# Performance work log

Hardware: AMD Instinct MI355X
Metric: run time of the kernel (lower is better)

Reference implementation:

```python
import jax, jax.numpy as jnp
from jax import lax
import numpy as np

L = 256       # regions
M = 8         # inputs
HID = 1024    # MLP hidden
T = 2048      # t_eval points
DT = 0.05
ALPHA_RES = 0.1
KAPPA, GAMMA, TAU, HALPHA, RHO, V0 = 0.65, 0.41, 0.98, 0.32, 0.34, 0.04


def setup_inputs() -> dict:
    key = jax.random.key(0)
    ks = jax.random.split(key, 8)
    A = -jnp.eye(L, dtype=jnp.float32) + 0.05 * jax.random.normal(ks[0], (L, L), jnp.float32) / np.sqrt(L)
    B = 0.01 * jax.random.normal(ks[1], (M, L, L), jnp.float32) / np.sqrt(L)
    C = 0.1 * jax.random.normal(ks[2], (L, M), jnp.float32)
    W1 = jax.random.normal(ks[3], (HID, L + M), jnp.float32) / np.sqrt(L + M)
    b1 = jnp.zeros((HID,), jnp.float32)
    W2 = jax.random.normal(ks[4], (L, HID), jnp.float32) / np.sqrt(HID)
    b2 = jnp.zeros((L,), jnp.float32)
    # u sampled on half-step grid: stages of step i use rows 2i, 2i+1, 2i+1, 2i+2
    u_seq = 0.1 * jax.random.uniform(ks[5], (2 * (T - 1) + 1, M), jnp.float32)
    t_eval = jnp.arange(T, dtype=jnp.float32) * DT
    return {"A": A, "B": B, "C": C, "W1": W1, "b1": b1, "W2": W2, "b2": b2,
            "u_seq": u_seq, "t_eval": t_eval}


def _simulate(A, B, C, W1, b1, W2, b2, u_seq, t_eval):
    l = A.shape[0]

    def dyn(state, u_t):
        z = state[:l]
        s_, f_, v_, q_ = state[l:].reshape(4, l)
        # residual MLP on concat(z, u)
        zu = jnp.concatenate([z, u_t])
        res = W2 @ jnp.tanh(W1 @ zu + b1) + b2
        # bilinear neuronal dynamics + residual
        dz = A @ z + jnp.einsum('m,mij,j->i', u_t, B, z) + C @ u_t + ALPHA_RES * res
        # hemodynamic balloon model
        ds = z - KAPPA * s_ - GAMMA * (f_ - 1.0)
        df = s_
        fv = v_ ** (1.0 / HALPHA)        # outflow v^(1/alpha)
        dv = (f_ - fv) / TAU
        E = 1.0 - (1.0 - RHO) ** (1.0 / f_)  # oxygen extraction
        dq = (f_ * E / RHO - fv * q_ / v_) / TAU
        return jnp.concatenate([dz, ds, df, dv, dq])

    def rk4_step(state, inp):
        h, u0, um, u1 = inp
        k1 = dyn(state, u0)
        k2 = dyn(state + 0.5 * h * k1, um)
        k3 = dyn(state + 0.5 * h * k2, um)
        k4 = dyn(state + h * k3, u1)
        nxt = state + (h / 6.0) * (k1 + 2.0 * k2 + 2.0 * k3 + k4)
        return nxt, nxt

    s0 = jnp.concatenate([jnp.zeros((2 * l,), A.dtype), jnp.ones((3 * l,), A.dtype)])  # z=0,s=0,f=v=q=1
    hs = t_eval[1:] - t_eval[:-1]                  # [T-1]
    u0 = u_seq[0:-2:2]; um = u_seq[1:-1:2]; u1 = u_seq[2::2]
    _, states = lax.scan(rk4_step, s0, (hs, u0, um, u1))
    S = jnp.concatenate([s0[None, :], states], axis=0)  # [T, 5l]
    v = S[:, 3 * l:4 * l]
    q = S[:, 4 * l:5 * l]
    k1b, k2b, k3b = 7.0 * RHO, 2.0, 2.0 * RHO - 0.2
    Y = V0 * (k1b * (1.0 - q) + k2b * (1.0 - q / v) + k3b * (1.0 - v))  # [T, l]
    return S, Y


def reference(A, B, C, W1, b1, W2, b2, u_seq, t_eval):
    return _simulate(A, B, C, W1, b1, W2, b2, u_seq, t_eval)
```

## Files before the change

### kernel.cpp

```cpp
#include <hip/hip_runtime.h>
#include <cmath>

#define LN 256
#define MM 8
#define HIDN 1024
#define NSTEP 2047
#define NWG 32
#define TPB 256
#define W1R 32
#define GR 8
#define ZUN (LN+MM)

#define KAPPA 0.65f
#define GAMMA 0.41f
#define TAUC 0.98f
#define INV_HALPHA 3.125f
#define RHOC 0.34f
#define V0C 0.04f
#define ALPHA 0.1f
#define LOG2_1MRHO (-0.5994620717f)

#define OFF_W1 0
#define N_W1 (W1R*ZUN)
#define OFF_W2 (OFF_W1+N_W1)
#define N_W2 (W1R*LN)
#define OFF_A (OFF_W2+N_W2)
#define N_A (GR*LN)
#define OFF_B (OFF_A+N_A)
#define N_B (MM*GR*LN)
#define OFF_C (OFF_B+N_B)
#define N_C (GR*MM)
#define OFF_B1 (OFF_C+N_C)
#define N_B1 (W1R)
#define OFF_B2 (OFF_B1+N_B1)
#define N_B2 (GR)
#define OFF_ZU (OFF_B2+N_B2)
#define N_ZU (ZUN)
#define OFF_H (OFF_ZU+N_ZU)
#define N_H (W1R)
#define OFF_P (OFF_H+N_H)
#define N_P (GR)
#define SMEM_FLOATS (OFF_P+N_P)
#define SMEM_BYTES (SMEM_FLOATS*4)

#define WS_PART_OFF 4096
#define FLG_STRIDE 16

__global__ void dcm_init(unsigned int* flg) {
  flg[threadIdx.x] = 0u;
}

__global__ void __launch_bounds__(TPB, 1) dcm_kernel(
    const float* __restrict__ Ag, const float* __restrict__ Bg,
    const float* __restrict__ Cg, const float* __restrict__ W1g,
    const float* __restrict__ b1g, const float* __restrict__ W2g,
    const float* __restrict__ b2g, const float* __restrict__ Ug,
    const float* __restrict__ Tg, float* __restrict__ outg,
    float* __restrict__ part, unsigned int* __restrict__ flg)
{
  extern __shared__ float sm[];
  const int wg = blockIdx.x, tid = threadIdx.x;
  float* w1s = sm + OFF_W1;
  float* w2s = sm + OFF_W2;
  float* as_ = sm + OFF_A;
  float* bs_ = sm + OFF_B;
  float* cs_ = sm + OFF_C;
  float* b1s = sm + OFF_B1;
  float* b2s = sm + OFF_B2;
  float* zu  = sm + OFF_ZU;
  float* hsh = sm + OFF_H;
  float* pts = sm + OFF_P;

  for (int i = tid; i < N_W1; i += TPB) {
    int r = i / ZUN, k = i - r * ZUN;
    w1s[i] = W1g[(wg * W1R + r) * ZUN + k];
  }
  for (int i = tid; i < N_W2; i += TPB) {
    int c = i >> 8, r = i & (LN - 1);
    w2s[i] = W2g[r * HIDN + wg * W1R + c];
  }
  for (int i = tid; i < N_A; i += TPB) {
    int r = i >> 8, k = i & (LN - 1);
    as_[i] = Ag[(wg * GR + r) * LN + k];
  }
  for (int i = tid; i < N_B; i += TPB) {
    int m = i / (GR * LN); int rem = i - m * GR * LN;
    int r = rem >> 8, k = rem & (LN - 1);
    bs_[i] = Bg[(m * LN + wg * GR + r) * LN + k];
  }
  for (int i = tid; i < N_C; i += TPB) {
    int r = i >> 3, m = i & 7;
    cs_[i] = Cg[(wg * GR + r) * MM + m];
  }
  for (int i = tid; i < N_B1; i += TPB) b1s[i] = b1g[wg * W1R + i];
  for (int i = tid; i < N_B2; i += TPB) b2s[i] = b2g[wg * GR + i];

  float zb = 0.f, sb = 0.f, fb = 1.f, vb = 1.f, qb = 1.f;
  zu[tid] = 0.f;

  if (wg == 0) {
    outg[tid] = 0.f;
    outg[LN + tid] = 0.f;
    outg[2 * LN + tid] = 1.f;
    outg[3 * LN + tid] = 1.f;
    outg[4 * LN + tid] = 1.f;
    outg[(size_t)2048 * 1280 + tid] = 0.f;
  }

  int pp = 0;

  for (int t = 0; t < NSTEP; ++t) {
    float hstep = Tg[t + 1] - Tg[t];
    float zst = zb, sst = sb, fst = fb, vst = vb, qst = qb;
    float kz = 0.f, ks = 0.f, kf = 0.f, kv = 0.f, kq = 0.f;

    for (int st = 0; st < 4; ++st) {
      int usel = (st == 0) ? (2 * t) : (st == 3) ? (2 * t + 2) : (2 * t + 1);
      if (tid < MM) zu[LN + tid] = Ug[usel * MM + tid];
      __syncthreads();

      float uu[MM];
      #pragma unroll
      for (int m = 0; m < MM; ++m) uu[m] = zu[LN + m];

      {
        int row = tid >> 3, sub = tid & 7;
        const float* wrow = w1s + row * ZUN + sub * 33;
        const float* zrow = zu + sub * 33;
        float acc = 0.f;
        #pragma unroll
        for (int j = 0; j < 33; ++j) acc += wrow[j] * zrow[j];
        acc += __shfl_xor(acc, 1);
        acc += __shfl_xor(acc, 2);
        acc += __shfl_xor(acc, 4);
        if (sub == 0) hsh[row] = tanhf(acc + b1s[row]);
      }
      {
        int grow = tid >> 5, gsub = tid & 31;
        const float* arow = as_ + grow * LN;
        float ga = 0.f;
        #pragma unroll
        for (int j = 0; j < 8; ++j) {
          int k = gsub + 32 * j;
          float w = arow[k];
          #pragma unroll
          for (int m = 0; m < MM; ++m) w += uu[m] * bs_[(m * GR + grow) * LN + k];
          ga += w * zu[k];
        }
        ga += __shfl_xor(ga, 1);
        ga += __shfl_xor(ga, 2);
        ga += __shfl_xor(ga, 4);
        ga += __shfl_xor(ga, 8);
        ga += __shfl_xor(ga, 16);
        if (gsub == 0) {
          float cu = 0.f;
          #pragma unroll
          for (int m = 0; m < MM; ++m) cu += cs_[grow * MM + m] * uu[m];
          pts[grow] = ga + cu + ALPHA * b2s[grow];
        }
      }
      __syncthreads();

      float pr;
      {
        float a2 = 0.f;
        #pragma unroll 8
        for (int c = 0; c < W1R; ++c) a2 += w2s[c * LN + tid] * hsh[c];
        pr = ALPHA * a2;
        int rl = tid - wg * GR;
        if (rl >= 0 && rl < GR) pr += pts[rl];
      }
      __hip_atomic_store(&part[((pp * NWG) + wg) * LN + tid], pr,
                         __ATOMIC_RELAXED, __HIP_MEMORY_SCOPE_AGENT);

      float ds = zst - KAPPA * sst - GAMMA * (fst - 1.f);
      float df = sst;
      float fv = exp2f(INV_HALPHA * log2f(vst));
      float dv = (fst - fv) / TAUC;
      float E  = 1.f - exp2f(LOG2_1MRHO / fst);
      float dq = (fst * E / RHOC - fv * qst / vst) / TAUC;

      __syncthreads();

      unsigned e = (unsigned)(4 * t + st + 1);
      if (tid == 0)
        __hip_atomic_store(&flg[wg * FLG_STRIDE], e,
                           __ATOMIC_RELAXED, __HIP_MEMORY_SCOPE_AGENT);

      {
        const unsigned* fp_ = &flg[(tid & 31) * FLG_STRIDE];
        for (;;) {
          unsigned v = __hip_atomic_load(fp_, __ATOMIC_RELAXED,
                                         __HIP_MEMORY_SCOPE_AGENT);
          if (__ballot(v >= e) == 0xFFFFFFFFFFFFFFFFull) break;
        }
      }

      float dz = 0.f;
      #pragma unroll
      for (int g = 0; g < NWG; ++g)
        dz += __hip_atomic_load(&part[(pp * NWG + g) * LN + tid],
                                __ATOMIC_RELAXED, __HIP_MEMORY_SCOPE_AGENT);

      float wk = (st == 0 || st == 3) ? 1.f : 2.f;
      kz += wk * dz; ks += wk * ds; kf += wk * df; kv += wk * dv; kq += wk * dq;

      if (st < 3) {
        float c = (st == 2) ? hstep : 0.5f * hstep;
        zst = zb + c * dz; sst = sb + c * ds; fst = fb + c * df;
        vst = vb + c * dv; qst = qb + c * dq;
        zu[tid] = zst;
      }
      pp ^= 1;
    }

    float h6 = hstep * (1.f / 6.f);
    zb += h6 * kz; sb += h6 * ks; fb += h6 * kf; vb += h6 * kv; qb += h6 * kq;
    zu[tid] = zb;

    if ((t & (NWG - 1)) == wg) {
      size_t ro = (size_t)(t + 1) * 1280;
      outg[ro + tid] = zb;
      outg[ro + LN + tid] = sb;
      outg[ro + 2 * LN + tid] = fb;
      outg[ro + 3 * LN + tid] = vb;
      outg[ro + 4 * LN + tid] = qb;
      float yv = V0C * (2.38f * (1.f - qb) + 2.f * (1.f - qb / vb) + 0.48f * (1.f - vb));
      outg[(size_t)2048 * 1280 + (size_t)(t + 1) * LN + tid] = yv;
    }
  }
}

extern "C" void kernel_launch(void* const* d_in, const int* in_sizes, int n_in,
                              void* d_out, int out_size, void* d_ws, size_t ws_size,
                              hipStream_t stream) {
  const float* Ag  = (const float*)d_in[0];
  const float* Bg  = (const float*)d_in[1];
  const float* Cg  = (const float*)d_in[2];
  const float* W1g = (const float*)d_in[3];
  const float* b1g = (const float*)d_in[4];
  const float* W2g = (const float*)d_in[5];
  const float* b2g = (const float*)d_in[6];
  const float* Ug  = (const float*)d_in[7];
  const float* Tg  = (const float*)d_in[8];
  float* outg = (float*)d_out;

  unsigned int* flg = (unsigned int*)d_ws;
  float* part = (float*)((char*)d_ws + WS_PART_OFF);

  hipFuncSetAttribute((const void*)dcm_kernel,
                      hipFuncAttributeMaxDynamicSharedMemorySize, SMEM_BYTES);

  hipLaunchKernelGGL(dcm_init, dim3(1), dim3(512), 0, stream, flg);
  hipLaunchKernelGGL(dcm_kernel, dim3(NWG), dim3(TPB), SMEM_BYTES, stream,
                     Ag, Bg, Cg, W1g, b1g, W2g, b2g, Ug, Tg, outg, part, flg);
}
```

Before: 27.70 ms.

## Pack epoch tags with partial sums to replace flag barrier

The inter-workgroup exchange now writes each partial sum together with its step epoch as a single 64-bit atomic store into a double-buffered array. Consumers poll the data slots directly until every tag matches, which removes the separate flag store, the extra __syncthreads, the ballot spin and the second round of loads. The flag-reset init kernel is dropped, and the three u rows for each step are loaded into registers once per step. In exchange, every thread polls 32 remote 64-bit slots, and correctness relies on stale workspace contents never carrying a matching epoch.

```diff
diff --git a/kernel.cpp b/kernel.cpp
--- a/kernel.cpp
+++ b/kernel.cpp
@@ -43,12 +43,6 @@
 #define SMEM_FLOATS (OFF_P+N_P)
 #define SMEM_BYTES (SMEM_FLOATS*4)
 
-#define WS_PART_OFF 4096
-#define FLG_STRIDE 16
-
-__global__ void dcm_init(unsigned int* flg) {
-  flg[threadIdx.x] = 0u;
-}
 
 __global__ void __launch_bounds__(TPB, 1) dcm_kernel(
     const float* __restrict__ Ag, const float* __restrict__ Bg,
@@ -56,7 +50,7 @@
     const float* __restrict__ b1g, const float* __restrict__ W2g,
     const float* __restrict__ b2g, const float* __restrict__ Ug,
     const float* __restrict__ Tg, float* __restrict__ outg,
-    float* __restrict__ part, unsigned int* __restrict__ flg)
+    unsigned long long* __restrict__ ex)
 {
   extern __shared__ float sm[];
   const int wg = blockIdx.x, tid = threadIdx.x;
@@ -107,16 +101,20 @@
     outg[(size_t)2048 * 1280 + tid] = 0.f;
   }
 
-  int pp = 0;
-
   for (int t = 0; t < NSTEP; ++t) {
     float hstep = Tg[t + 1] - Tg[t];
     float zst = zb, sst = sb, fst = fb, vst = vb, qst = qb;
     float kz = 0.f, ks = 0.f, kf = 0.f, kv = 0.f, kq = 0.f;
 
+    float u0r = 0.f, umr = 0.f, u1r = 0.f;
+    if (tid < MM) {
+      u0r = Ug[(2 * t) * MM + tid];
+      umr = Ug[(2 * t + 1) * MM + tid];
+      u1r = Ug[(2 * t + 2) * MM + tid];
+    }
+
     for (int st = 0; st < 4; ++st) {
-      int usel = (st == 0) ? (2 * t) : (st == 3) ? (2 * t + 2) : (2 * t + 1);
-      if (tid < MM) zu[LN + tid] = Ug[usel * MM + tid];
+      if (tid < MM) zu[LN + tid] = (st == 0) ? u0r : (st == 3) ? u1r : umr;
       __syncthreads();
 
       float uu[MM];
@@ -170,7 +168,11 @@
         int rl = tid - wg * GR;
         if (rl >= 0 && rl < GR) pr += pts[rl];
       }
-      __hip_atomic_store(&part[((pp * NWG) + wg) * LN + tid], pr,
+
+      const unsigned e = (unsigned)(4 * t + st + 1);
+      unsigned long long* exb = ex + (size_t)(e & 1) * (NWG * LN);
+      __hip_atomic_store(&exb[wg * LN + tid],
+                         ((unsigned long long)e << 32) | (unsigned long long)__float_as_uint(pr),
                          __ATOMIC_RELAXED, __HIP_MEMORY_SCOPE_AGENT);
 
       float ds = zst - KAPPA * sst - GAMMA * (fst - 1.f);
@@ -180,27 +182,24 @@
       float E  = 1.f - exp2f(LOG2_1MRHO / fst);
       float dq = (fst * E / RHOC - fv * qst / vst) / TAUC;
 
-      __syncthreads();
-
-      unsigned e = (unsigned)(4 * t + st + 1);
-      if (tid == 0)
-        __hip_atomic_store(&flg[wg * FLG_STRIDE], e,
-                           __ATOMIC_RELAXED, __HIP_MEMORY_SCOPE_AGENT);
-
-      {
-        const unsigned* fp_ = &flg[(tid & 31) * FLG_STRIDE];
-        for (;;) {
-          unsigned v = __hip_atomic_load(fp_, __ATOMIC_RELAXED,
-                                         __HIP_MEMORY_SCOPE_AGENT);
-          if (__ballot(v >= e) == 0xFFFFFFFFFFFFFFFFull) break;
-        }
+      unsigned long long vv[NWG];
+      unsigned done = 0u;
+      while (done != 0xFFFFFFFFu) {
+        #pragma unroll
+        for (int g = 0; g < NWG; ++g)
+          if (!(done & (1u << g)))
+            vv[g] = __hip_atomic_load(&exb[g * LN + tid],
+                                      __ATOMIC_RELAXED, __HIP_MEMORY_SCOPE_AGENT);
+        #pragma unroll
+        for (int g = 0; g < NWG; ++g)
+          if (!(done & (1u << g)))
+            if ((unsigned)(vv[g] >> 32) == e) done |= (1u << g);
       }
 
       float dz = 0.f;
       #pragma unroll
       for (int g = 0; g < NWG; ++g)
-        dz += __hip_atomic_load(&part[(pp * NWG + g) * LN + tid],
-                                __ATOMIC_RELAXED, __HIP_MEMORY_SCOPE_AGENT);
+        dz += __uint_as_float((unsigned)vv[g]);
 
       float wk = (st == 0 || st == 3) ? 1.f : 2.f;
       kz += wk * dz; ks += wk * ds; kf += wk * df; kv += wk * dv; kq += wk * dq;
@@ -211,7 +210,6 @@
         vst = vb + c * dv; qst = qb + c * dq;
         zu[tid] = zst;
       }
-      pp ^= 1;
     }
 
     float h6 = hstep * (1.f / 6.f);
@@ -245,13 +243,11 @@
   const float* Tg  = (const float*)d_in[8];
   float* outg = (float*)d_out;
 
-  unsigned int* flg = (unsigned int*)d_ws;
-  float* part = (float*)((char*)d_ws + WS_PART_OFF);
+  unsigned long long* ex = (unsigned long long*)d_ws;
 
   hipFuncSetAttribute((const void*)dcm_kernel,
                       hipFuncAttributeMaxDynamicSharedMemorySize, SMEM_BYTES);
 
-  hipLaunchKernelGGL(dcm_init, dim3(1), dim3(512), 0, stream, flg);
   hipLaunchKernelGGL(dcm_kernel, dim3(NWG), dim3(TPB), SMEM_BYTES, stream,
-                     Ag, Bg, Cg, W1g, b1g, W2g, b2g, Ug, Tg, outg, part, flg);
+                     Ag, Bg, Cg, W1g, b1g, W2g, b2g, Ug, Tg, outg, ex);
 }
```

Measured after the change: 43.60 ms. +57.4%, slower.

## Use per-wavefront release flags and double-buffered z to drop a block barrier

Applied to the files above, without the earlier changes.

Each wavefront now publishes its own release flag and waits only on the matching wavefront flags of the other workgroups. This removes the block-wide __syncthreads before the inter-workgroup handshake. The z/u shared buffer is double-buffered so stage writes cannot race with reads from the previous stage. The u loads are hoisted out of the stage loop and the partial-sum reduction is split into two accumulators. A deadman spin limit is added, which can silently break out of the wait and produce wrong results if a workgroup stalls for too long.

```diff
diff --git a/kernel.cpp b/kernel.cpp
--- a/kernel.cpp
+++ b/kernel.cpp
@@ -19,6 +19,8 @@
 #define V0C 0.04f
 #define ALPHA 0.1f
 #define LOG2_1MRHO (-0.5994620717f)
+
+#define DEADMAN (1<<14)
 
 #define OFF_W1 0
 #define N_W1 (W1R*ZUN)
@@ -34,20 +36,18 @@
 #define N_B1 (W1R)
 #define OFF_B2 (OFF_B1+N_B1)
 #define N_B2 (GR)
-#define OFF_ZU (OFF_B2+N_B2)
-#define N_ZU (ZUN)
-#define OFF_H (OFF_ZU+N_ZU)
-#define N_H (W1R)
-#define OFF_P (OFF_H+N_H)
-#define N_P (GR)
-#define SMEM_FLOATS (OFF_P+N_P)
+#define OFF_ZA (OFF_B2+N_B2)
+#define OFF_ZB (OFF_ZA+ZUN)
+#define OFF_H (OFF_ZB+ZUN)
+#define OFF_P (OFF_H+W1R)
+#define SMEM_FLOATS (OFF_P+GR)
 #define SMEM_BYTES (SMEM_FLOATS*4)
 
-#define WS_PART_OFF 4096
-#define FLG_STRIDE 16
-
-__global__ void dcm_init(unsigned int* flg) {
-  flg[threadIdx.x] = 0u;
+#define WS_PART_OFF 8192
+#define FSTR 16
+
+__global__ void dcm_init(unsigned* wflag) {
+  for (int i = threadIdx.x; i < NWG * 4 * FSTR; i += 256) wflag[i] = 0u;
 }
 
 __global__ void __launch_bounds__(TPB, 1) dcm_kernel(
@@ -56,10 +56,11 @@
     const float* __restrict__ b1g, const float* __restrict__ W2g,
     const float* __restrict__ b2g, const float* __restrict__ Ug,
     const float* __restrict__ Tg, float* __restrict__ outg,
-    float* __restrict__ part, unsigned int* __restrict__ flg)
+    float* __restrict__ part, unsigned* __restrict__ wflag)
 {
   extern __shared__ float sm[];
   const int wg = blockIdx.x, tid = threadIdx.x;
+  const int myw = tid >> 6;
   float* w1s = sm + OFF_W1;
   float* w2s = sm + OFF_W2;
   float* as_ = sm + OFF_A;
@@ -67,7 +68,8 @@
   float* cs_ = sm + OFF_C;
   float* b1s = sm + OFF_B1;
   float* b2s = sm + OFF_B2;
-  float* zu  = sm + OFF_ZU;
+  float* zA  = sm + OFF_ZA;
+  float* zB  = sm + OFF_ZB;
   float* hsh = sm + OFF_H;
   float* pts = sm + OFF_P;
 
@@ -96,7 +98,7 @@
   for (int i = tid; i < N_B2; i += TPB) b2s[i] = b2g[wg * GR + i];
 
   float zb = 0.f, sb = 0.f, fb = 1.f, vb = 1.f, qb = 1.f;
-  zu[tid] = 0.f;
+  zA[tid] = 0.f;
 
   if (wg == 0) {
     outg[tid] = 0.f;
@@ -107,26 +109,36 @@
     outg[(size_t)2048 * 1280 + tid] = 0.f;
   }
 
-  int pp = 0;
-
   for (int t = 0; t < NSTEP; ++t) {
     float hstep = Tg[t + 1] - Tg[t];
     float zst = zb, sst = sb, fst = fb, vst = vb, qst = qb;
     float kz = 0.f, ks = 0.f, kf = 0.f, kv = 0.f, kq = 0.f;
 
+    float u0r = 0.f, umr = 0.f, u1r = 0.f;
+    if (tid < MM) {
+      u0r = Ug[(2 * t) * MM + tid];
+      umr = Ug[(2 * t + 1) * MM + tid];
+      u1r = Ug[(2 * t + 2) * MM + tid];
+    }
+
     for (int st = 0; st < 4; ++st) {
-      int usel = (st == 0) ? (2 * t) : (st == 3) ? (2 * t + 2) : (2 * t + 1);
-      if (tid < MM) zu[LN + tid] = Ug[usel * MM + tid];
+      const int stg = 4 * t + st;
+      const unsigned fl = (unsigned)stg + 1;
+      float* zcur = (st & 1) ? zB : zA;
+      float* znxt = (st & 1) ? zA : zB;
+      float* pslot = part + (size_t)(stg & 1) * (NWG * LN);
+
+      if (tid < MM) zcur[LN + tid] = (st == 0) ? u0r : (st == 3) ? u1r : umr;
       __syncthreads();
 
       float uu[MM];
       #pragma unroll
-      for (int m = 0; m < MM; ++m) uu[m] = zu[LN + m];
+      for (int m = 0; m < MM; ++m) uu[m] = zcur[LN + m];
 
       {
         int row = tid >> 3, sub = tid & 7;
         const float* wrow = w1s + row * ZUN + sub * 33;
-        const float* zrow = zu + sub * 33;
+        const float* zrow = zcur + sub * 33;
         float acc = 0.f;
         #pragma unroll
         for (int j = 0; j < 33; ++j) acc += wrow[j] * zrow[j];
@@ -145,7 +157,7 @@
           float w = arow[k];
           #pragma unroll
           for (int m = 0; m < MM; ++m) w += uu[m] * bs_[(m * GR + grow) * LN + k];
-          ga += w * zu[k];
+          ga += w * zcur[k];
         }
         ga += __shfl_xor(ga, 1);
         ga += __shfl_xor(ga, 2);
@@ -161,17 +173,16 @@
       }
       __syncthreads();
 
-      float pr;
       {
         float a2 = 0.f;
         #pragma unroll 8
         for (int c = 0; c < W1R; ++c) a2 += w2s[c * LN + tid] * hsh[c];
-        pr = ALPHA * a2;
+        float pr = ALPHA * a2;
         int rl = tid - wg * GR;
         if (rl >= 0 && rl < GR) pr += pts[rl];
-      }
-      __hip_atomic_store(&part[((pp * NWG) + wg) * LN + tid], pr,
-                         __ATOMIC_RELAXED, __HIP_MEMORY_SCOPE_AGENT);
+        __hip_atomic_store(&pslot[wg * LN + tid], pr,
+                           __ATOMIC_RELAXED, __HIP_MEMORY_SCOPE_AGENT);
+      }
 
       float ds = zst - KAPPA * sst - GAMMA * (fst - 1.f);
       float df = sst;
@@ -180,27 +191,30 @@
       float E  = 1.f - exp2f(LOG2_1MRHO / fst);
       float dq = (fst * E / RHOC - fv * qst / vst) / TAUC;
 
-      __syncthreads();
-
-      unsigned e = (unsigned)(4 * t + st + 1);
-      if (tid == 0)
-        __hip_atomic_store(&flg[wg * FLG_STRIDE], e,
-                           __ATOMIC_RELAXED, __HIP_MEMORY_SCOPE_AGENT);
-
-      {
-        const unsigned* fp_ = &flg[(tid & 31) * FLG_STRIDE];
+      if ((tid & 63) == 0)
+        __hip_atomic_store(&wflag[(wg * 4 + myw) * FSTR], fl,
+                           __ATOMIC_RELEASE, __HIP_MEMORY_SCOPE_AGENT);
+
+      {
+        const unsigned* fp_ = &wflag[((tid & 31) * 4 + myw) * FSTR];
+        int spins = 0;
         for (;;) {
           unsigned v = __hip_atomic_load(fp_, __ATOMIC_RELAXED,
                                          __HIP_MEMORY_SCOPE_AGENT);
-          if (__ballot(v >= e) == 0xFFFFFFFFFFFFFFFFull) break;
+          if (__ballot(v >= fl) == 0xFFFFFFFFFFFFFFFFull) break;
+          if (++spins > DEADMAN) break;
         }
       }
 
-      float dz = 0.f;
+      float dza = 0.f, dzb2 = 0.f;
       #pragma unroll
-      for (int g = 0; g < NWG; ++g)
-        dz += __hip_atomic_load(&part[(pp * NWG + g) * LN + tid],
-                                __ATOMIC_RELAXED, __HIP_MEMORY_SCOPE_AGENT);
+      for (int g = 0; g < NWG; g += 2) {
+        dza  += __hip_atomic_load(&pslot[g * LN + tid],
+                                  __ATOMIC_RELAXED, __HIP_MEMORY_SCOPE_AGENT);
+        dzb2 += __hip_atomic_load(&pslot[(g + 1) * LN + tid],
+                                  __ATOMIC_RELAXED, __HIP_MEMORY_SCOPE_AGENT);
+      }
+      float dz = dza + dzb2;
 
       float wk = (st == 0 || st == 3) ? 1.f : 2.f;
       kz += wk * dz; ks += wk * ds; kf += wk * df; kv += wk * dv; kq += wk * dq;
@@ -209,14 +223,13 @@
         float c = (st == 2) ? hstep : 0.5f * hstep;
         zst = zb + c * dz; sst = sb + c * ds; fst = fb + c * df;
         vst = vb + c * dv; qst = qb + c * dq;
-        zu[tid] = zst;
-      }
-      pp ^= 1;
+        znxt[tid] = zst;
+      }
     }
 
     float h6 = hstep * (1.f / 6.f);
     zb += h6 * kz; sb += h6 * ks; fb += h6 * kf; vb += h6 * kv; qb += h6 * kq;
-    zu[tid] = zb;
+    zA[tid] = zb;
 
     if ((t & (NWG - 1)) == wg) {
       size_t ro = (size_t)(t + 1) * 1280;
@@ -245,13 +258,13 @@
   const float* Tg  = (const float*)d_in[8];
   float* outg = (float*)d_out;
 
-  unsigned int* flg = (unsigned int*)d_ws;
+  unsigned* wflag = (unsigned*)d_ws;
   float* part = (float*)((char*)d_ws + WS_PART_OFF);
 
   hipFuncSetAttribute((const void*)dcm_kernel,
                       hipFuncAttributeMaxDynamicSharedMemorySize, SMEM_BYTES);
 
-  hipLaunchKernelGGL(dcm_init, dim3(1), dim3(512), 0, stream, flg);
+  hipLaunchKernelGGL(dcm_init, dim3(1), dim3(256), 0, stream, wflag);
   hipLaunchKernelGGL(dcm_kernel, dim3(NWG), dim3(TPB), SMEM_BYTES, stream,
-                     Ag, Bg, Cg, W1g, b1g, W2g, b2g, Ug, Tg, outg, part, flg);
+                     Ag, Bg, Cg, W1g, b1g, W2g, b2g, Ug, Tg, outg, part, wflag);
 }
```

After: 46.10 ms. +66.4%, slower.
